# Optimization experiments

Hardware: AMD Instinct MI355X
Metric: run time of the kernel (lower is better)

## Reference

```python
import jax, jax.numpy as jnp
import numpy as np

EMBED = 1024
HEADS = 16
HEAD_DIM = EMBED // HEADS
HIDDEN = 4096
EPS = 1e-5


def setup_inputs() -> dict:
    key = jax.random.key(0)
    ks = jax.random.split(key, 12)
    s_e = 1.0 / np.sqrt(EMBED)
    s_h = 1.0 / np.sqrt(HIDDEN)
    inp = {
        'x': jax.random.normal(ks[0], (2, 2048, EMBED), jnp.float32),
        'Wq': jax.random.uniform(ks[1], (EMBED, EMBED), jnp.float32, -s_e, s_e),
        'bq': jnp.zeros((EMBED,), jnp.float32),
        'Wk': jax.random.uniform(ks[2], (EMBED, EMBED), jnp.float32, -s_e, s_e),
        'bk': jnp.zeros((EMBED,), jnp.float32),
        'Wv': jax.random.uniform(ks[3], (EMBED, EMBED), jnp.float32, -s_e, s_e),
        'bv': jnp.zeros((EMBED,), jnp.float32),
        'Wo': jax.random.uniform(ks[4], (EMBED, EMBED), jnp.float32, -s_e, s_e),
        'bo': jnp.zeros((EMBED,), jnp.float32),
        'g1': jnp.ones((EMBED,), jnp.float32),
        'b1': jnp.zeros((EMBED,), jnp.float32),
        'W1': jax.random.uniform(ks[5], (EMBED, HIDDEN), jnp.float32, -s_e, s_e),
        'bm1': jnp.zeros((HIDDEN,), jnp.float32),
        'W2': jax.random.uniform(ks[6], (HIDDEN, EMBED), jnp.float32, -s_h, s_h),
        'bm2': jnp.zeros((EMBED,), jnp.float32),
        'g2': jnp.ones((EMBED,), jnp.float32),
        'b2': jnp.zeros((EMBED,), jnp.float32),
    }
    return inp


def _layernorm(x, g, b):
    mu = jnp.mean(x, axis=-1, keepdims=True)
    var = jnp.mean(jnp.square(x - mu), axis=-1, keepdims=True)
    return (x - mu) * jax.lax.rsqrt(var + EPS) * g + b


def _attention(x, Wq, bq, Wk, bk, Wv, bv, Wo, bo):
    b, n, d = x.shape
    def split(h):  # [b,n,d] -> [b,H,n,hd]
        return h.reshape(b, n, HEADS, HEAD_DIM).transpose(0, 2, 1, 3)
    q = split(x @ Wq + bq)
    k = split(x @ Wk + bk)
    v = split(x @ Wv + bv)
    # NOTE: original multiplies by sqrt(head_dim) (bug preserved for faithfulness)
    scores = jnp.einsum('bhqd,bhkd->bhqk', q, k) * jnp.sqrt(jnp.float32(HEAD_DIM))
    causal = jnp.tril(jnp.ones((n, n), bool))
    scores = jnp.where(causal, scores, -jnp.inf)
    attn = jax.nn.softmax(scores, axis=-1)
    out = jnp.einsum('bhqk,bhkd->bhqd', attn, v)
    out = out.transpose(0, 2, 1, 3).reshape(b, n, d)
    return out @ Wo + bo


def reference(x, Wq, bq, Wk, bk, Wv, bv, Wo, bo, g1, b1, W1, bm1, W2, bm2, g2, b2):
    res1 = x
    x = _layernorm(_attention(x, Wq, bq, Wk, bk, Wv, bv, Wo, bo), g1, b1) + res1
    res2 = x
    h = jax.nn.gelu(x @ W1 + bm1, approximate=False) @ W2 + bm2
    return _layernorm(h, g2, b2) + res2
```

## Files before the change

### kernel.cpp

```cpp
#include <hip/hip_runtime.h>
#include <stdint.h>

typedef unsigned short u16;
typedef short short8 __attribute__((ext_vector_type(8)));
typedef float f32x4 __attribute__((ext_vector_type(4)));
typedef u16 u16x4 __attribute__((ext_vector_type(4)));
typedef u16 u16x8 __attribute__((ext_vector_type(8)));

#define MODE_F32  0
#define MODE_GELU 2
#define MODE_VT   4

#define QSCALE 11.5415603271f

__device__ __forceinline__ float b2f(u16 v) {
    union { uint32_t u; float f; } x; x.u = ((uint32_t)v) << 16; return x.f;
}
__device__ __forceinline__ u16 f2b(float f) {
    union { float f; uint32_t u; } x; x.f = f;
    uint32_t u = x.u;
    return (u16)((u + 0x7FFFu + ((u >> 16) & 1u)) >> 16);
}

#define ASYNC16(gp, lp)                                                        \
    __builtin_amdgcn_global_load_lds(                                          \
        (const __attribute__((address_space(1))) uint32_t*)(const void*)(gp),  \
        (__attribute__((address_space(3))) uint32_t*)(void*)(lp), 16, 0, 0)

#define MFMA16(a, b, c) __builtin_amdgcn_mfma_f32_16x16x32_bf16((a), (b), (c), 0, 0, 0)

__global__ __launch_bounds__(256) void split_f32(
    const float* __restrict__ in, u16* __restrict__ hi, u16* __restrict__ lo)
{
    const int i = (blockIdx.x * 256 + threadIdx.x) * 4;
    f32x4 v = *(const f32x4*)&in[i];
    u16x4 h, l;
    for (int k = 0; k < 4; k++) {
        h[k] = f2b(v[k]);
        l[k] = f2b(v[k] - b2f(h[k]));
    }
    *(u16x4*)&hi[i] = h;
    *(u16x4*)&lo[i] = l;
}

__global__ __launch_bounds__(256) void transpose_f32_bf16(
    const float* __restrict__ in, u16* __restrict__ out, int rows, int cols)
{
    __shared__ float t[32][33];
    const int r0 = blockIdx.y * 32, c0 = blockIdx.x * 32;
    const int tr = threadIdx.x >> 3, tc = (threadIdx.x & 7) * 4;
    f32x4 v = *(const f32x4*)&in[(size_t)(r0 + tr) * cols + c0 + tc];
    for (int i = 0; i < 4; i++) t[tr][tc + i] = v[i];
    __syncthreads();
    u16x4 ov;
    for (int i = 0; i < 4; i++) ov[i] = f2b(t[tc + i][tr]);
    *(u16x4*)&out[(size_t)(c0 + tr) * rows + r0 + tc] = ov;
}

__global__ __launch_bounds__(256) void transpose_split_f32(
    const float* __restrict__ in, u16* __restrict__ hi, u16* __restrict__ lo,
    int rows, int cols)
{
    __shared__ float t[32][33];
    const int r0 = blockIdx.y * 32, c0 = blockIdx.x * 32;
    const int tr = threadIdx.x >> 3, tc = (threadIdx.x & 7) * 4;
    f32x4 v = *(const f32x4*)&in[(size_t)(r0 + tr) * cols + c0 + tc];
    for (int i = 0; i < 4; i++) t[tr][tc + i] = v[i];
    __syncthreads();
    u16x4 hv, lv;
    for (int i = 0; i < 4; i++) {
        const float f = t[tc + i][tr];
        hv[i] = f2b(f);
        lv[i] = f2b(f - b2f(hv[i]));
    }
    const size_t o = (size_t)(c0 + tr) * rows + r0 + tc;
    *(u16x4*)&hi[o] = hv;
    *(u16x4*)&lo[o] = lv;
}

__global__ __launch_bounds__(256) void gemm_qk_x3(
    const u16* __restrict__ Ahi, const u16* __restrict__ Alo,
    const u16* __restrict__ Bhi, const u16* __restrict__ Blo,
    const float* __restrict__ bq, const float* __restrict__ bk,
    u16* __restrict__ Qhi, u16* __restrict__ Qlo,
    u16* __restrict__ Khi, u16* __restrict__ Klo)
{
    const int K = 1024;
    __shared__ __align__(16) u16 SM[32768];
    u16* lAh = SM;          u16* lAl = SM + 8192;
    u16* lBh = SM + 16384;  u16* lBl = SM + 24576;

    const int tid = threadIdx.x;
    const int w = tid >> 6, lane = tid & 63;
    const int lane15 = lane & 15, q = lane >> 4;
    const int tM = blockIdx.y * 128, tN = blockIdx.x * 128;
    const int m0 = (w >> 1) * 64, n0 = (w & 1) * 64;

    f32x4 acc[4][4];
    for (int i = 0; i < 4; i++)
        for (int j = 0; j < 4; j++)
            acc[i][j] = (f32x4){0.f, 0.f, 0.f, 0.f};

    const int pa0 = 2 * w, pa1 = 2 * w + 1;
    const int srow = lane >> 2, sch = lane & 3;
    const u16* Ah = Ahi + (size_t)tM * K;
    const u16* Al = Alo + (size_t)tM * K;
    const u16* Bh = Bhi + (size_t)tN * K;
    const u16* Bl = Blo + (size_t)tN * K;
    const size_t r0 = (size_t)(pa0 * 16 + srow) * K + sch * 8;
    const size_t r1 = (size_t)(pa1 * 16 + srow) * K + sch * 8;

    ASYNC16(Ah + r0, lAh + pa0 * 512);  ASYNC16(Ah + r1, lAh + pa1 * 512);
    ASYNC16(Al + r0, lAl + pa0 * 512);  ASYNC16(Al + r1, lAl + pa1 * 512);
    ASYNC16(Bh + r0, lBh + pa0 * 512);  ASYNC16(Bh + r1, lBh + pa1 * 512);
    ASYNC16(Bl + r0, lBl + pa0 * 512);  ASYNC16(Bl + r1, lBl + pa1 * 512);

    const int NT = K / 32;
    for (int kt = 0; kt < NT; kt++) {
        __syncthreads();
        const int cb = (kt & 1) * 4096, nb = 4096 - cb;
        if (kt + 1 < NT) {
            const int k0 = (kt + 1) * 32;
            ASYNC16(Ah + r0 + k0, lAh + nb + pa0 * 512);  ASYNC16(Ah + r1 + k0, lAh + nb + pa1 * 512);
            ASYNC16(Al + r0 + k0, lAl + nb + pa0 * 512);  ASYNC16(Al + r1 + k0, lAl + nb + pa1 * 512);
            ASYNC16(Bh + r0 + k0, lBh + nb + pa0 * 512);  ASYNC16(Bh + r1 + k0, lBh + nb + pa1 * 512);
            ASYNC16(Bl + r0 + k0, lBl + nb + pa0 * 512);  ASYNC16(Bl + r1 + k0, lBl + nb + pa1 * 512);
        }
        short8 afh[4], afl[4], bfh[4], bfl[4];
        for (int i = 0; i < 4; i++) {
            const int o = cb + (m0 + i * 16 + lane15) * 32 + q * 8;
            afh[i] = *(const short8*)&lAh[o];
            afl[i] = *(const short8*)&lAl[o];
        }
        for (int j = 0; j < 4; j++) {
            const int o = cb + (n0 + j * 16 + lane15) * 32 + q * 8;
            bfh[j] = *(const short8*)&lBh[o];
            bfl[j] = *(const short8*)&lBl[o];
        }
        for (int i = 0; i < 4; i++)
            for (int j = 0; j < 4; j++) {
                acc[i][j] = MFMA16(afh[i], bfh[j], acc[i][j]);
                acc[i][j] = MFMA16(afh[i], bfl[j], acc[i][j]);
                acc[i][j] = MFMA16(afl[i], bfh[j], acc[i][j]);
            }
    }

    const bool isQ = (tN < 1024);
    u16* dhi = isQ ? Qhi : Khi;
    u16* dlo = isQ ? Qlo : Klo;
    const int cN = isQ ? tN : (tN - 1024);
    const float scl = isQ ? QSCALE : 1.0f;
    u16* sC = SM;
    for (int pass = 0; pass < 2; pass++) {
        __syncthreads();
        for (int i = 0; i < 4; i++) {
            const int rl0 = m0 + i * 16 + q * 4;
            for (int j = 0; j < 4; j++) {
                const int cl = n0 + j * 16 + lane15;
                const float bv = isQ ? bq[cN + cl] : bk[cN + cl];
                for (int r = 0; r < 4; r++) {
                    const float v = (acc[i][j][r] + bv) * scl;
                    const u16 hv = f2b(v);
                    sC[(rl0 + r) * 136 + cl] = pass == 0 ? hv : f2b(v - b2f(hv));
                }
            }
        }
        __syncthreads();
        u16* dst = pass == 0 ? dhi : dlo;
        for (int t8 = 0; t8 < 8; t8++) {
            const int rl = t8 * 16 + (tid >> 4), cl = (tid & 15) * 8;
            *(u16x8*)&dst[(size_t)(tM + rl) * 1024 + cN + cl] = *(const u16x8*)&sC[rl * 136 + cl];
        }
    }
}

__global__ __launch_bounds__(256) void gemm_bt(
    const u16* __restrict__ A, const u16* __restrict__ Bt, const float* __restrict__ bias,
    int M, int N, int K, int mode,
    float* __restrict__ outF, u16* __restrict__ outB, size_t pstride)
{
    __shared__ __align__(16) u16 SM[17408];
    u16* lA = SM;
    u16* lB = SM + 8192;

    const int tid = threadIdx.x;
    const int w = tid >> 6, lane = tid & 63;
    const int lane15 = lane & 15, q = lane >> 4;
    const int tM = blockIdx.y * 128, tN = blockIdx.x * 128;
    const int m0 = (w >> 1) * 64, n0 = (w & 1) * 64;

    const int kchunk = K / gridDim.z;
    const int koff = blockIdx.z * kchunk;
    outF += (size_t)blockIdx.z * pstride;

    f32x4 acc[4][4];
    for (int i = 0; i < 4; i++)
        for (int j = 0; j < 4; j++)
            acc[i][j] = (f32x4){0.f, 0.f, 0.f, 0.f};

    const int pa0 = 2 * w, pa1 = 2 * w + 1;
    const int srow = lane >> 2, sch = lane & 3;
    const u16* Abase = A + (size_t)tM * K + koff;
    const u16* Bbase = Bt + (size_t)tN * K + koff;
    const size_t r0 = (size_t)(pa0 * 16 + srow) * K + sch * 8;
    const size_t r1 = (size_t)(pa1 * 16 + srow) * K + sch * 8;

    ASYNC16(Abase + r0, lA + pa0 * 512);
    ASYNC16(Abase + r1, lA + pa1 * 512);
    ASYNC16(Bbase + r0, lB + pa0 * 512);
    ASYNC16(Bbase + r1, lB + pa1 * 512);

    const int NT = kchunk / 32;
    for (int kt = 0; kt < NT; kt++) {
        __syncthreads();
        const int cb = (kt & 1) * 4096, nb = 4096 - cb;
        if (kt + 1 < NT) {
            const int k0 = (kt + 1) * 32;
            ASYNC16(Abase + r0 + k0, lA + nb + pa0 * 512);
            ASYNC16(Abase + r1 + k0, lA + nb + pa1 * 512);
            ASYNC16(Bbase + r0 + k0, lB + nb + pa0 * 512);
            ASYNC16(Bbase + r1 + k0, lB + nb + pa1 * 512);
        }
        short8 af[4], bf[4];
        for (int i = 0; i < 4; i++) af[i] = *(const short8*)&lA[cb + (m0 + i * 16 + lane15) * 32 + q * 8];
        for (int j = 0; j < 4; j++) bf[j] = *(const short8*)&lB[cb + (n0 + j * 16 + lane15) * 32 + q * 8];
        for (int i = 0; i < 4; i++)
            for (int j = 0; j < 4; j++)
                acc[i][j] = MFMA16(af[i], bf[j], acc[i][j]);
    }

    if (mode == MODE_F32) {
        for (int i = 0; i < 4; i++) {
            const int rb = tM + m0 + i * 16 + q * 4;
            for (int j = 0; j < 4; j++) {
                const int col = tN + n0 + j * 16 + lane15;
                const float bv = (bias && blockIdx.z == 0) ? bias[col] : 0.f;
                for (int r = 0; r < 4; r++)
                    outF[(size_t)(rb + r) * N + col] = acc[i][j][r] + bv;
            }
        }
        return;
    }

    u16* sC = SM;
    __syncthreads();
    if (mode == MODE_GELU) {
        for (int i = 0; i < 4; i++) {
            const int rl0 = m0 + i * 16 + q * 4;
            for (int j = 0; j < 4; j++) {
                const int cl = n0 + j * 16 + lane15;
                const float bv = bias[tN + cl];
                for (int r = 0; r < 4; r++) {
                    float v = acc[i][j][r] + bv;
                    v = 0.5f * v * (1.f + erff(v * 0.70710678118f));
                    sC[(rl0 + r) * 136 + cl] = f2b(v);
                }
            }
        }
        __syncthreads();
        for (int t8 = 0; t8 < 8; t8++) {
            const int rl = t8 * 16 + (tid >> 4), cl = (tid & 15) * 8;
            *(u16x8*)&outB[(size_t)(tM + rl) * N + tN + cl] = *(const u16x8*)&sC[rl * 136 + cl];
        }
    } else {
        for (int i = 0; i < 4; i++) {
            const int rl0 = m0 + i * 16 + q * 4;
            for (int j = 0; j < 4; j++) {
                const int cl = n0 + j * 16 + lane15;
                const float bv = bias[tN + cl];
                for (int r = 0; r < 4; r++)
                    sC[cl * 136 + rl0 + r] = f2b(acc[i][j][r] + bv);
            }
        }
        __syncthreads();
        const int bb = tM >> 11, nbase = tM & 2047;
        for (int t8 = 0; t8 < 8; t8++) {
            const int cl = t8 * 16 + (tid >> 4), rl = (tid & 15) * 8;
            const int colg = tN + cl;
            u16* dst = &outB[((size_t)(bb * 16 + (colg >> 6)) * 64 + (colg & 63)) * 2048 + nbase + rl];
            *(u16x8*)dst = *(const u16x8*)&sC[cl * 136 + rl];
        }
    }
}

__global__ __launch_bounds__(256) void attn_fwd(
    const u16* __restrict__ Qhig, const u16* __restrict__ Qlog,
    const u16* __restrict__ Khig, const u16* __restrict__ Klog,
    const u16* __restrict__ Vtg, u16* __restrict__ Og)
{
    __shared__ u16 lQh[2][2048], lQl[2][2048];
    __shared__ u16 lKh[2][2][1024], lKl[2][2][1024];
    __shared__ u16 lV[2][2048];
    __shared__ u16 lP[4][640];

    const int tid = threadIdx.x, w = tid >> 6, lane = tid & 63;
    const int lane15 = lane & 15, q = lane >> 4;
    const int bh = blockIdx.x & 31;
    const int qb = 31 - (blockIdx.x >> 5);
    const int b = bh >> 4, h = bh & 15;

    const size_t xoff = (size_t)b * 2048 * 1024 + h * 64;
    const u16* Qh_ = Qhig + xoff;
    const u16* Ql_ = Qlog + xoff;
    const u16* Kh_ = Khig + xoff;
    const u16* Kl_ = Klog + xoff;
    const u16* Vbh = Vtg + (size_t)bh * 64 * 2048;
    u16* Obh = Og + xoff;

    const int srow = lane >> 2, sch = lane & 3;
    const float NEG = -3.0e38f;
    const int qrow0 = qb * 64;
    const int ntiles = 2 * qb + 2;

    for (int ii = 0; ii < 4; ii++) {
        const int id = w * 4 + ii;
        const int idq = id & 7, ks = idq >> 2, p = idq & 3;
        const size_t so = (size_t)(qrow0 + p * 16 + srow) * 1024 + ks * 32 + sch * 8;
        if (id < 8) ASYNC16(Qh_ + so, &lQh[ks][p * 512]);
        else        ASYNC16(Ql_ + so, &lQl[ks][p * 512]);
    }
    for (int ii = 0; ii < 3; ii++) {
        const int id = w * 3 + ii;
        if (id < 8) {
            const int sel = id >> 2, idk = id & 3, ks = idk >> 1, hh = idk & 1;
            const size_t so = (size_t)(hh * 16 + srow) * 1024 + ks * 32 + sch * 8;
            if (sel == 0) ASYNC16(Kh_ + so, &lKh[0][ks][hh * 512]);
            else          ASYNC16(Kl_ + so, &lKl[0][ks][hh * 512]);
        } else {
            const int p = id - 8;
            ASYNC16(Vbh + (size_t)(p * 16 + srow) * 2048 + sch * 8, &lV[0][p * 512]);
        }
    }

    f32x4 o[4];
    for (int j = 0; j < 4; j++) o[j] = (f32x4){0.f, 0.f, 0.f, 0.f};
    float mrow[4], lrow[4];
    for (int r = 0; r < 4; r++) { mrow[r] = NEG; lrow[r] = 0.f; }
    short8 aqh0 = {}, aqh1 = {}, aql0 = {}, aql1 = {};
    bool first = true;

    for (int t = 0; t < ntiles; t++) {
        __syncthreads();
        const int cur = t & 1, nxt = cur ^ 1;
        if (t + 1 < ntiles) {
            const int kk1 = (t + 1) * 32;
            for (int ii = 0; ii < 3; ii++) {
                const int id = w * 3 + ii;
                if (id < 8) {
                    const int sel = id >> 2, idk = id & 3, ks = idk >> 1, hh = idk & 1;
                    const size_t so = (size_t)(kk1 + hh * 16 + srow) * 1024 + ks * 32 + sch * 8;
                    if (sel == 0) ASYNC16(Kh_ + so, &lKh[nxt][ks][hh * 512]);
                    else          ASYNC16(Kl_ + so, &lKl[nxt][ks][hh * 512]);
                } else {
                    const int p = id - 8;
                    ASYNC16(Vbh + (size_t)(p * 16 + srow) * 2048 + kk1 + sch * 8,
                            &lV[nxt][p * 512]);
                }
            }
        }
        if (first) {
            const int o0 = (w * 16 + lane15) * 32 + q * 8;
            aqh0 = *(const short8*)&lQh[0][o0];
            aqh1 = *(const short8*)&lQh[1][o0];
            aql0 = *(const short8*)&lQl[0][o0];
            aql1 = *(const short8*)&lQl[1][o0];
            first = false;
        }
        const int kk0 = t * 32;
        f32x4 s[2];
        for (int sub = 0; sub < 2; sub++) {
            const int ko = (sub * 16 + lane15) * 32 + q * 8;
            short8 bkh0 = *(const short8*)&lKh[cur][0][ko];
            short8 bkh1 = *(const short8*)&lKh[cur][1][ko];
            short8 bkl0 = *(const short8*)&lKl[cur][0][ko];
            short8 bkl1 = *(const short8*)&lKl[cur][1][ko];
            f32x4 z = (f32x4){0.f, 0.f, 0.f, 0.f};
            z = MFMA16(aqh0, bkh0, z);
            z = MFMA16(aqh1, bkh1, z);
            z = MFMA16(aqh0, bkl0, z);
            z = MFMA16(aqh1, bkl1, z);
            z = MFMA16(aql0, bkh0, z);
            z = MFMA16(aql1, bkh1, z);
            s[sub] = z;
        }
        const int rbase = qrow0 + w * 16 + q * 4;
        for (int sub = 0; sub < 2; sub++)
            for (int r = 0; r < 4; r++) {
                const int key = kk0 + sub * 16 + lane15;
                if (key > rbase + r) s[sub][r] = NEG;
            }
        float mx[4];
        for (int r = 0; r < 4; r++) mx[r] = fmaxf(s[0][r], s[1][r]);
        for (int d = 1; d < 16; d <<= 1)
            for (int r = 0; r < 4; r++) mx[r] = fmaxf(mx[r], __shfl_xor(mx[r], d));
        float alpha[4];
        for (int r = 0; r < 4; r++) {
            const float mnew = fmaxf(mrow[r], mx[r]);
            alpha[r] = __builtin_exp2f(mrow[r] - mnew);
            mrow[r] = mnew;
        }
        float rsum[4] = {0.f, 0.f, 0.f, 0.f};
        for (int sub = 0; sub < 2; sub++)
            for (int r = 0; r < 4; r++) {
                const float p = __builtin_exp2f(s[sub][r] - mrow[r]);
                rsum[r] += p;
                lP[w][(q * 4 + r) * 40 + sub * 16 + lane15] = f2b(p);
            }
        for (int d = 1; d < 16; d <<= 1)
            for (int r = 0; r < 4; r++) rsum[r] += __shfl_xor(rsum[r], d);
        for (int r = 0; r < 4; r++) lrow[r] = lrow[r] * alpha[r] + rsum[r];
        for (int j = 0; j < 4; j++)
            for (int r = 0; r < 4; r++) o[j][r] *= alpha[r];
        short8 ap = *(const short8*)&lP[w][lane15 * 40 + q * 8];
        for (int j = 0; j < 4; j++) {
            short8 bv = *(const short8*)&lV[cur][(j * 16 + lane15) * 32 + q * 8];
            o[j] = MFMA16(ap, bv, o[j]);
        }
    }
    float inv[4];
    for (int r = 0; r < 4; r++) inv[r] = 1.0f / lrow[r];
    for (int j = 0; j < 4; j++)
        for (int r = 0; r < 4; r++)
            Obh[(size_t)(qrow0 + w * 16 + q * 4 + r) * 1024 + j * 16 + lane15] =
                f2b(o[j][r] * inv[r]);
}

__global__ __launch_bounds__(256) void ln_res(
    const float* __restrict__ Xa, const float* __restrict__ Xb,
    const float* __restrict__ resF, const u16* __restrict__ resB,
    const float* __restrict__ g, const float* __restrict__ bb,
    u16* __restrict__ outB, float* __restrict__ outF)
{
    const int w = threadIdx.x >> 6, lane = threadIdx.x & 63;
    const int row = blockIdx.x * 4 + w;
    const size_t rowo = (size_t)row * 1024;
    f32x4 v[4];
    float s = 0.f, ss = 0.f;
    for (int i = 0; i < 4; i++) {
        const int c0 = (i * 64 + lane) * 4;
        v[i] = *(const f32x4*)&Xa[rowo + c0];
        if (Xb) {
            f32x4 v2 = *(const f32x4*)&Xb[rowo + c0];
            for (int k = 0; k < 4; k++) v[i][k] += v2[k];
        }
        for (int k = 0; k < 4; k++) { s += v[i][k]; ss += v[i][k] * v[i][k]; }
    }
    for (int d = 1; d < 64; d <<= 1) { s += __shfl_xor(s, d); ss += __shfl_xor(ss, d); }
    const float mu = s * (1.f / 1024.f);
    const float var = ss * (1.f / 1024.f) - mu * mu;
    const float rstd = rsqrtf(var + 1e-5f);
    for (int i = 0; i < 4; i++) {
        const int c0 = (i * 64 + lane) * 4;
        f32x4 gv = *(const f32x4*)&g[c0];
        f32x4 bv = *(const f32x4*)&bb[c0];
        f32x4 rv;
        if (resF) rv = *(const f32x4*)&resF[rowo + c0];
        else {
            u16x4 rb = *(const u16x4*)&resB[rowo + c0];
            for (int k = 0; k < 4; k++) rv[k] = b2f(rb[k]);
        }
        f32x4 ov;
        for (int k = 0; k < 4; k++)
            ov[k] = (v[i][k] - mu) * rstd * gv[k] + bv[k] + rv[k];
        if (outF) *(f32x4*)&outF[rowo + c0] = ov;
        if (outB) {
            u16x4 ob;
            for (int k = 0; k < 4; k++) ob[k] = f2b(ov[k]);
            *(u16x4*)&outB[rowo + c0] = ob;
        }
    }
}

extern "C" void kernel_launch(void* const* d_in, const int* in_sizes, int n_in,
                              void* d_out, int out_size, void* d_ws, size_t ws_size,
                              hipStream_t stream)
{
    const float* x   = (const float*)d_in[0];
    const float* Wq  = (const float*)d_in[1];  const float* bq  = (const float*)d_in[2];
    const float* Wk  = (const float*)d_in[3];  const float* bk  = (const float*)d_in[4];
    const float* Wv  = (const float*)d_in[5];  const float* bv  = (const float*)d_in[6];
    const float* Wo  = (const float*)d_in[7];  const float* bo  = (const float*)d_in[8];
    const float* g1  = (const float*)d_in[9];  const float* b1  = (const float*)d_in[10];
    const float* W1  = (const float*)d_in[11]; const float* bm1 = (const float*)d_in[12];
    const float* W2  = (const float*)d_in[13]; const float* bm2 = (const float*)d_in[14];
    const float* g2  = (const float*)d_in[15]; const float* b2  = (const float*)d_in[16];

    const size_t MB = (size_t)1 << 20;
    char* ws = (char*)d_ws;
    u16* xhi    = (u16*)(ws + 0 * MB);
    u16* xlo    = (u16*)(ws + 8 * MB);
    u16* WqkThi = (u16*)(ws + 16 * MB);
    u16* WqkTlo = (u16*)(ws + 20 * MB);
    u16* WvT    = (u16*)(ws + 24 * MB);
    u16* WoT    = (u16*)(ws + 26 * MB);
    u16* W1T    = (u16*)(ws + 32 * MB);
    u16* W2T    = (u16*)(ws + 40 * MB);
    u16* Qhi    = (u16*)(ws + 48 * MB);
    u16* Qlo    = (u16*)(ws + 56 * MB);
    u16* Khi    = (u16*)(ws + 64 * MB);
    u16* Klo    = (u16*)(ws + 72 * MB);
    u16* Vtb    = (u16*)(ws + 80 * MB);
    u16* aout   = (u16*)(ws + 16 * MB);
    float* O1   = (float*)(ws + 48 * MB);
    float* O2   = (float*)(ws + 64 * MB);
    u16* x1b    = (u16*)(ws + 80 * MB);
    u16* Hb     = (u16*)(ws + 0 * MB);
    float* H2a  = (float*)(ws + 48 * MB);
    float* H2b  = (float*)(ws + 64 * MB);

    split_f32<<<4096, 256, 0, stream>>>(x, xhi, xlo);
    transpose_split_f32<<<dim3(32, 32), 256, 0, stream>>>(Wq, WqkThi, WqkTlo, 1024, 1024);
    transpose_split_f32<<<dim3(32, 32), 256, 0, stream>>>(Wk, WqkThi + 1024 * 1024,
                                                          WqkTlo + 1024 * 1024, 1024, 1024);
    transpose_f32_bf16<<<dim3(32, 32), 256, 0, stream>>>(Wv, WvT, 1024, 1024);
    transpose_f32_bf16<<<dim3(32, 32), 256, 0, stream>>>(Wo, WoT, 1024, 1024);
    transpose_f32_bf16<<<dim3(128, 32), 256, 0, stream>>>(W1, W1T, 1024, 4096);
    transpose_f32_bf16<<<dim3(32, 128), 256, 0, stream>>>(W2, W2T, 4096, 1024);

    gemm_qk_x3<<<dim3(16, 32), 256, 0, stream>>>(xhi, xlo, WqkThi, WqkTlo, bq, bk,
                                                 Qhi, Qlo, Khi, Klo);
    gemm_bt<<<dim3(8, 32), 256, 0, stream>>>(xhi, WvT, bv, 4096, 1024, 1024,
                                             MODE_VT, nullptr, Vtb, 0);

    attn_fwd<<<dim3(1024), 256, 0, stream>>>(Qhi, Qlo, Khi, Klo, Vtb, aout);

    gemm_bt<<<dim3(8, 32, 2), 256, 0, stream>>>(aout, WoT, bo, 4096, 1024, 1024,
                                                MODE_F32, O1, nullptr, (size_t)16 * MB / 4);
    ln_res<<<1024, 256, 0, stream>>>(O1, O2, x, nullptr, g1, b1, x1b, nullptr);

    gemm_bt<<<dim3(32, 32), 256, 0, stream>>>(x1b, W1T, bm1, 4096, 4096, 1024,
                                              MODE_GELU, nullptr, Hb, 0);
    gemm_bt<<<dim3(8, 32, 2), 256, 0, stream>>>(Hb, W2T, bm2, 4096, 1024, 4096,
                                                MODE_F32, H2a, nullptr, (size_t)16 * MB / 4);
    ln_res<<<1024, 256, 0, stream>>>(H2a, H2b, nullptr, x1b, g2, b2, nullptr, (float*)d_out);
}
```

Measured before the change: 475.5 us.

## Skip fully masked key tiles per wave, compute row sums via MFMA, merge transposes

In attention, each wave now skips key tiles lying entirely above its own 16 causal rows and applies the causal mask only on diagonal tiles. Row sums of P come from an MFMA against a ones vector instead of shuffle reductions, P is rounded to bf16 by truncation, and the P scratch buffer reuses the Q shared-memory region (extra barrier after loading Q). Weight-transpose launches are merged pairwise via blockIdx.z to reduce launch count. Truncation slightly changes numerics, and the per-wave skip leaves waves in a block with unequal work.

Measured after the change: 472.0 us. About the same (-0.7%).

```diff
diff --git a/kernel.cpp b/kernel.cpp
--- a/kernel.cpp
+++ b/kernel.cpp
@@ -20,6 +20,10 @@
     union { float f; uint32_t u; } x; x.f = f;
     uint32_t u = x.u;
     return (u16)((u + 0x7FFFu + ((u >> 16) & 1u)) >> 16);
+}
+__device__ __forceinline__ u16 f2b_trunc(float f) {
+    union { float f; uint32_t u; } x; x.f = f;
+    return (u16)(x.u >> 16);
 }
 
 #define ASYNC16(gp, lp)                                                        \
@@ -44,8 +48,11 @@
 }
 
 __global__ __launch_bounds__(256) void transpose_f32_bf16(
-    const float* __restrict__ in, u16* __restrict__ out, int rows, int cols)
-{
+    const float* __restrict__ inA, u16* __restrict__ outA,
+    const float* __restrict__ inB, u16* __restrict__ outB, int rows, int cols)
+{
+    const float* in = blockIdx.z ? inB : inA;
+    u16* out = blockIdx.z ? outB : outA;
     __shared__ float t[32][33];
     const int r0 = blockIdx.y * 32, c0 = blockIdx.x * 32;
     const int tr = threadIdx.x >> 3, tc = (threadIdx.x & 7) * 4;
@@ -58,9 +65,13 @@
 }
 
 __global__ __launch_bounds__(256) void transpose_split_f32(
-    const float* __restrict__ in, u16* __restrict__ hi, u16* __restrict__ lo,
+    const float* __restrict__ inA, u16* __restrict__ hiA, u16* __restrict__ loA,
+    const float* __restrict__ inB, u16* __restrict__ hiB, u16* __restrict__ loB,
     int rows, int cols)
 {
+    const float* in = blockIdx.z ? inB : inA;
+    u16* hi = blockIdx.z ? hiB : hiA;
+    u16* lo = blockIdx.z ? loB : loA;
     __shared__ float t[32][33];
     const int r0 = blockIdx.y * 32, c0 = blockIdx.x * 32;
     const int tr = threadIdx.x >> 3, tc = (threadIdx.x & 7) * 4;
@@ -291,7 +302,6 @@
     __shared__ u16 lQh[2][2048], lQl[2][2048];
     __shared__ u16 lKh[2][2][1024], lKl[2][2][1024];
     __shared__ u16 lV[2][2048];
-    __shared__ u16 lP[4][640];
 
     const int tid = threadIdx.x, w = tid >> 6, lane = tid & 63;
     const int lane15 = lane & 15, q = lane >> 4;
@@ -307,10 +317,16 @@
     const u16* Vbh = Vtg + (size_t)bh * 64 * 2048;
     u16* Obh = Og + xoff;
 
+    u16* lP = &lQh[0][0] + w * 640;
+
     const int srow = lane >> 2, sch = lane & 3;
     const float NEG = -3.0e38f;
     const int qrow0 = qb * 64;
+    const int wrow0 = qrow0 + w * 16;
     const int ntiles = 2 * qb + 2;
+
+    short8 ones;
+    for (int i = 0; i < 8; i++) ones[i] = (short)0x3F80;
 
     for (int ii = 0; ii < 4; ii++) {
         const int id = w * 4 + ii;
@@ -337,11 +353,18 @@
     float mrow[4], lrow[4];
     for (int r = 0; r < 4; r++) { mrow[r] = NEG; lrow[r] = 0.f; }
     short8 aqh0 = {}, aqh1 = {}, aql0 = {}, aql1 = {};
-    bool first = true;
 
     for (int t = 0; t < ntiles; t++) {
         __syncthreads();
         const int cur = t & 1, nxt = cur ^ 1;
+        if (t == 0) {
+            const int o0 = (w * 16 + lane15) * 32 + q * 8;
+            aqh0 = *(const short8*)&lQh[0][o0];
+            aqh1 = *(const short8*)&lQh[1][o0];
+            aql0 = *(const short8*)&lQl[0][o0];
+            aql1 = *(const short8*)&lQl[1][o0];
+            __syncthreads();
+        }
         if (t + 1 < ntiles) {
             const int kk1 = (t + 1) * 32;
             for (int ii = 0; ii < 3; ii++) {
@@ -358,15 +381,9 @@
                 }
             }
         }
-        if (first) {
-            const int o0 = (w * 16 + lane15) * 32 + q * 8;
-            aqh0 = *(const short8*)&lQh[0][o0];
-            aqh1 = *(const short8*)&lQh[1][o0];
-            aql0 = *(const short8*)&lQl[0][o0];
-            aql1 = *(const short8*)&lQl[1][o0];
-            first = false;
-        }
         const int kk0 = t * 32;
+        if (kk0 > wrow0 + 15) continue;
+
         f32x4 s[2];
         for (int sub = 0; sub < 2; sub++) {
             const int ko = (sub * 16 + lane15) * 32 + q * 8;
@@ -383,12 +400,14 @@
             z = MFMA16(aql1, bkh1, z);
             s[sub] = z;
         }
-        const int rbase = qrow0 + w * 16 + q * 4;
-        for (int sub = 0; sub < 2; sub++)
-            for (int r = 0; r < 4; r++) {
-                const int key = kk0 + sub * 16 + lane15;
-                if (key > rbase + r) s[sub][r] = NEG;
-            }
+        const int rbase = wrow0 + q * 4;
+        if (kk0 + 31 > wrow0) {
+            for (int sub = 0; sub < 2; sub++)
+                for (int r = 0; r < 4; r++) {
+                    const int key = kk0 + sub * 16 + lane15;
+                    if (key > rbase + r) s[sub][r] = NEG;
+                }
+        }
         float mx[4];
         for (int r = 0; r < 4; r++) mx[r] = fmaxf(s[0][r], s[1][r]);
         for (int d = 1; d < 16; d <<= 1)
@@ -399,19 +418,17 @@
             alpha[r] = __builtin_exp2f(mrow[r] - mnew);
             mrow[r] = mnew;
         }
-        float rsum[4] = {0.f, 0.f, 0.f, 0.f};
         for (int sub = 0; sub < 2; sub++)
             for (int r = 0; r < 4; r++) {
                 const float p = __builtin_exp2f(s[sub][r] - mrow[r]);
-                rsum[r] += p;
-                lP[w][(q * 4 + r) * 40 + sub * 16 + lane15] = f2b(p);
-            }
-        for (int d = 1; d < 16; d <<= 1)
-            for (int r = 0; r < 4; r++) rsum[r] += __shfl_xor(rsum[r], d);
-        for (int r = 0; r < 4; r++) lrow[r] = lrow[r] * alpha[r] + rsum[r];
+                lP[(q * 4 + r) * 40 + sub * 16 + lane15] = f2b_trunc(p);
+            }
+        short8 ap = *(const short8*)&lP[lane15 * 40 + q * 8];
+        f32x4 zs = (f32x4){0.f, 0.f, 0.f, 0.f};
+        zs = MFMA16(ap, ones, zs);
+        for (int r = 0; r < 4; r++) lrow[r] = lrow[r] * alpha[r] + zs[r];
         for (int j = 0; j < 4; j++)
             for (int r = 0; r < 4; r++) o[j][r] *= alpha[r];
-        short8 ap = *(const short8*)&lP[w][lane15 * 40 + q * 8];
         for (int j = 0; j < 4; j++) {
             short8 bv = *(const short8*)&lV[cur][(j * 16 + lane15) * 32 + q * 8];
             o[j] = MFMA16(ap, bv, o[j]);
@@ -509,13 +526,12 @@
     float* H2b  = (float*)(ws + 64 * MB);
 
     split_f32<<<4096, 256, 0, stream>>>(x, xhi, xlo);
-    transpose_split_f32<<<dim3(32, 32), 256, 0, stream>>>(Wq, WqkThi, WqkTlo, 1024, 1024);
-    transpose_split_f32<<<dim3(32, 32), 256, 0, stream>>>(Wk, WqkThi + 1024 * 1024,
-                                                          WqkTlo + 1024 * 1024, 1024, 1024);
-    transpose_f32_bf16<<<dim3(32, 32), 256, 0, stream>>>(Wv, WvT, 1024, 1024);
-    transpose_f32_bf16<<<dim3(32, 32), 256, 0, stream>>>(Wo, WoT, 1024, 1024);
-    transpose_f32_bf16<<<dim3(128, 32), 256, 0, stream>>>(W1, W1T, 1024, 4096);
-    transpose_f32_bf16<<<dim3(32, 128), 256, 0, stream>>>(W2, W2T, 4096, 1024);
+    transpose_split_f32<<<dim3(32, 32, 2), 256, 0, stream>>>(
+        Wq, WqkThi, WqkTlo,
+        Wk, WqkThi + 1024 * 1024, WqkTlo + 1024 * 1024, 1024, 1024);
+    transpose_f32_bf16<<<dim3(32, 32, 2), 256, 0, stream>>>(Wv, WvT, Wo, WoT, 1024, 1024);
+    transpose_f32_bf16<<<dim3(128, 32), 256, 0, stream>>>(W1, W1T, nullptr, nullptr, 1024, 4096);
+    transpose_f32_bf16<<<dim3(32, 128), 256, 0, stream>>>(W2, W2T, nullptr, nullptr, 4096, 1024);
 
     gemm_qk_x3<<<dim3(16, 32), 256, 0, stream>>>(xhi, xlo, WqkThi, WqkTlo, bq, bk,
                                                  Qhi, Qlo, Khi, Klo);
```
